# Optimization experiments

Hardware: AMD Instinct MI355X
Metric: run time of the kernel (lower is better)

The kernel has to match this reference:

```python
import jax, jax.numpy as jnp
import numpy as np

N = 200000
E = 500000
F_IN = 165
HID = 256
N_CLASSES = 2


def setup_inputs() -> dict:
    key = jax.random.key(0)
    ks = jax.random.split(key, 8)
    x = jax.random.normal(ks[0], (N, F_IN), dtype=jnp.float32)
    edge_index = jax.random.randint(ks[1], (2, E), 0, N, dtype=jnp.int64)
    # PyG SAGEConv params: lin_l applied to mean-aggregated neighbors (with bias),
    # lin_r applied to root features (no bias). Glorot-ish init scale.
    def lin(k, fin, fout):
        return jax.random.normal(k, (fin, fout), dtype=jnp.float32) / np.sqrt(fin)
    return {
        "x": x,
        "edge_index": edge_index,
        "w1_l": lin(ks[2], F_IN, HID),
        "w1_r": lin(ks[3], F_IN, HID),
        "b1": jnp.zeros((HID,), dtype=jnp.float32),
        "w2_l": lin(ks[4], HID, N_CLASSES),
        "w2_r": lin(ks[5], HID, N_CLASSES),
        "b2": jnp.zeros((N_CLASSES,), dtype=jnp.float32),
    }


def _sage_conv(x, edge_index, w_l, w_r, b):
    # PyG SAGEConv with default mean aggregation:
    #   out = lin_l(mean_{j in N(i)} x_j) + lin_r(x_i) + b
    src, dst = edge_index[0], edge_index[1]
    n = x.shape[0]
    deg = jax.ops.segment_sum(jnp.ones((src.shape[0],), x.dtype), dst, num_segments=n)
    agg = jax.ops.segment_sum(x[src], dst, num_segments=n)  # [N, F]
    agg = agg / jnp.maximum(deg, 1.0)[:, None]
    return agg @ w_l + x @ w_r + b


def reference(x, edge_index, w1_l, w1_r, b1, w2_l, w2_r, b2):
    h = jax.nn.relu(_sage_conv(x, edge_index, w1_l, w1_r, b1))
    # F.dropout(training=self.training) is identity in eval mode.
    logits = _sage_conv(h, edge_index, w2_l, w2_r, b2)
    return (logits, edge_index)
```

## Files before the change

kernel.cpp:

```cpp
#include <hip/hip_runtime.h>
#include <hip/hip_bf16.h>
#include <hip/hip_fp16.h>

#define N_NODES 200000
#define N_EDGES 500000
#define F_IN    165
#define HID     256
#define SX      192
#define NB      782

typedef float    floatx4 __attribute__((ext_vector_type(4)));
typedef float    floatx4a __attribute__((ext_vector_type(4), aligned(16)));
typedef float    float4u __attribute__((ext_vector_type(4), aligned(4)));
typedef _Float16 half8   __attribute__((ext_vector_type(8)));

__global__ void cast_x_kernel(const float* __restrict__ x, half8* __restrict__ xh8) {
    int idx = blockIdx.x * blockDim.x + threadIdx.x;
    int row = idx / 24;
    int p = idx - row * 24;
    int f0 = p * 8;
    const float* px = x + (long)row * F_IN + f0;
    half8 r;
    if (f0 + 8 <= F_IN) {
        float4u lo = *(const float4u*)px;
        float4u hi = *(const float4u*)(px + 4);
#pragma unroll
        for (int q = 0; q < 4; ++q) r[q] = (_Float16)lo[q];
#pragma unroll
        for (int q = 0; q < 4; ++q) r[4 + q] = (_Float16)hi[q];
    } else {
#pragma unroll
        for (int q = 0; q < 8; ++q)
            r[q] = (f0 + q < F_IN) ? (_Float16)px[q] : (_Float16)0.0f;
    }
    xh8[idx] = r;
}

__global__ void hist_kernel(const int* __restrict__ ei, int* __restrict__ degi) {
    int e = blockIdx.x * blockDim.x + threadIdx.x;
    if (e < N_EDGES) atomicAdd(&degi[ei[N_EDGES + e]], 1);
}

__global__ __launch_bounds__(256) void block_sum_kernel(const int* __restrict__ degi,
                                                        int* __restrict__ bsum) {
    __shared__ int sh[256];
    int t = threadIdx.x, i = blockIdx.x * 256 + t;
    sh[t] = (i < N_NODES) ? degi[i] : 0;
    __syncthreads();
#pragma unroll
    for (int off = 128; off > 0; off >>= 1) {
        if (t < off) sh[t] += sh[t + off];
        __syncthreads();
    }
    if (t == 0) bsum[blockIdx.x] = sh[0];
}

__global__ __launch_bounds__(1024) void scan_bsum_kernel(const int* __restrict__ bsum,
                                                         int* __restrict__ boff,
                                                         int* __restrict__ row_start) {
    __shared__ int sh[1024];
    int t = threadIdx.x;
    int v = (t < NB) ? bsum[t] : 0;
    sh[t] = v;
    __syncthreads();
    for (int off = 1; off < 1024; off <<= 1) {
        int u = (t >= off) ? sh[t - off] : 0;
        __syncthreads();
        sh[t] += u;
        __syncthreads();
    }
    if (t < NB) boff[t] = sh[t] - v;
    if (t == 1023) row_start[N_NODES] = sh[1023];
}

__global__ __launch_bounds__(256) void scan_emit_kernel(const int* __restrict__ degi,
                                                        const int* __restrict__ boff,
                                                        int* __restrict__ row_start,
                                                        int* __restrict__ cursor,
                                                        float* __restrict__ invdeg) {
    __shared__ int sh[256];
    int t = threadIdx.x, i = blockIdx.x * 256 + t;
    int d = (i < N_NODES) ? degi[i] : 0;
    sh[t] = d;
    __syncthreads();
#pragma unroll
    for (int off = 1; off < 256; off <<= 1) {
        int u = (t >= off) ? sh[t - off] : 0;
        __syncthreads();
        sh[t] += u;
        __syncthreads();
    }
    if (i < N_NODES) {
        int row = boff[blockIdx.x] + sh[t] - d;
        row_start[i] = row;
        cursor[i] = row;
        invdeg[i] = 1.0f / fmaxf((float)d, 1.0f);
    }
}

__global__ void scatter_edges_kernel(const int* __restrict__ ei,
                                     int* __restrict__ cursor,
                                     int* __restrict__ csr) {
    int e = blockIdx.x * blockDim.x + threadIdx.x;
    if (e >= N_EDGES) return;
    int s = ei[e];
    int d = ei[N_EDGES + e];
    int pos = atomicAdd(&cursor[d], 1);
    csr[pos] = s;
}

__global__ void gather_agg_kernel(const half8* __restrict__ xh8,
                                  const int* __restrict__ row_start,
                                  const int* __restrict__ csr,
                                  half8* __restrict__ aggh8) {
    int idx = blockIdx.x * blockDim.x + threadIdx.x;
    int n = idx / 24;
    int p = idx - n * 24;
    int e0 = row_start[n], e1 = row_start[n + 1];
    half8 acc = {0, 0, 0, 0, 0, 0, 0, 0};
    half8 acc2 = {0, 0, 0, 0, 0, 0, 0, 0};
    int e = e0;
    for (; e + 2 <= e1; e += 2) {
        int s0 = csr[e], s1 = csr[e + 1];
        half8 v0 = xh8[(long)s0 * 24 + p];
        half8 v1 = xh8[(long)s1 * 24 + p];
        acc += v0;
        acc2 += v1;
    }
    if (e < e1) acc += xh8[(long)csr[e] * 24 + p];
    aggh8[idx] = acc + acc2;
}

__global__ void prep_bfrag_kernel(const float* __restrict__ w1l,
                                  const float* __restrict__ w1r,
                                  _Float16* __restrict__ bfrag) {
    int gid = blockIdx.x * blockDim.x + threadIdx.x;
    if (gid >= 12 * 16 * 64) return;
    int lane = gid & 63;
    int j = (gid >> 6) & 15;
    int c = gid >> 10;
    int quad = lane >> 4, n = lane & 15;
    const float* w = (c < 6) ? w1l : w1r;
    int kb = (c < 6 ? c : c - 6) * 32;
    int col = j * 16 + n;
    half8 r;
#pragma unroll
    for (int q = 0; q < 8; ++q) {
        int k = kb + quad * 8 + q;
        r[q] = (_Float16)((k < F_IN) ? w[k * HID + col] : 0.0f);
    }
    *(half8*)(bfrag + gid * 8) = r;
}

__global__ __launch_bounds__(512, 2) void gemm_fused_kernel(
        const _Float16* __restrict__ xh, const _Float16* __restrict__ aggh,
        const float* __restrict__ invdeg, const _Float16* __restrict__ bfrag,
        const float* __restrict__ b1,
        const float* __restrict__ w2l, const float* __restrict__ w2r,
        float* __restrict__ tl, float* __restrict__ tr) {
    __shared__ __attribute__((aligned(16))) _Float16 As[2][128 * 32];
    __shared__ float tlr[128][4];
    const int tid = threadIdx.x;
    const int w = tid >> 6, lane = tid & 63;
    const int quad = lane >> 4, l15 = lane & 15;
    const int rowbase = blockIdx.x * 128;
    const int mrow0 = rowbase + (w & 1) * 64;
    const int rhalf = (w & 1) * 64;
    const int jbase = (w >> 1) * 4;

    ((float*)tlr)[tid < 512 ? tid : 0] = 0.0f;

    const int srow_l = tid >> 2;
    const int sseg = (tid & 3) ^ ((srow_l >> 1) & 3);
    int srow = rowbase + srow_l;
    if (srow >= N_NODES) srow = N_NODES - 1;
    const long sgoff = (long)srow * SX + sseg * 8;

    floatx4 acc[4][4];
#pragma unroll
    for (int i = 0; i < 4; ++i)
#pragma unroll
        for (int jj = 0; jj < 4; ++jj)
            acc[i][jj] = (floatx4){0.f, 0.f, 0.f, 0.f};

    __syncthreads();

#pragma unroll 1
    for (int it = 0; it < 6; ++it) {
#pragma unroll
        for (int u = 0; u < 2; ++u) {
            const int cc = it * 2 + u;
            const _Float16* __restrict__ src = (cc < 6) ? aggh : xh;
            const int kb = (cc < 6 ? cc : cc - 6) * 32;
            const _Float16* gp = src + sgoff + kb;
            char* dst = (char*)(&As[u][0]) + (tid & ~63) * 16;
            __builtin_amdgcn_global_load_lds(
                (const __attribute__((address_space(1))) void*)gp,
                (__attribute__((address_space(3))) void*)dst, 16, 0, 0);
        }
        __syncthreads();

#pragma unroll
        for (int u = 0; u < 2; ++u) {
            const int cc = it * 2 + u;
            half8 a[4], b[4];
#pragma unroll
            for (int i = 0; i < 4; ++i) {
                int r = rhalf + i * 16 + l15;
                int slot = r * 4 + (quad ^ ((r >> 1) & 3));
                a[i] = *(const half8*)(&As[u][slot * 8]);
            }
#pragma unroll
            for (int jj = 0; jj < 4; ++jj)
                b[jj] = *(const half8*)(bfrag + (((cc * 16) + jbase + jj) * 64 + lane) * 8);
#pragma unroll
            for (int i = 0; i < 4; ++i)
#pragma unroll
                for (int jj = 0; jj < 4; ++jj)
                    acc[i][jj] = __builtin_amdgcn_mfma_f32_16x16x32_f16(a[i], b[jj], acc[i][jj], 0, 0, 0);

            if (cc == 5) {
#pragma unroll
                for (int i = 0; i < 4; ++i) {
                    int rb = mrow0 + i * 16 + quad * 4;
                    floatx4 iv;
                    if (rb + 3 < N_NODES) {
                        iv = *(const floatx4a*)(invdeg + rb);
                    } else {
#pragma unroll
                        for (int t = 0; t < 4; ++t)
                            iv[t] = (rb + t < N_NODES) ? invdeg[rb + t] : 0.0f;
                    }
#pragma unroll
                    for (int jj = 0; jj < 4; ++jj)
                        acc[i][jj] *= iv;
                }
            }
        }
        __syncthreads();
    }

    float bb[4], wl0[4], wl1[4], wr0[4], wr1[4];
#pragma unroll
    for (int jj = 0; jj < 4; ++jj) {
        int col = (w >> 1) * 64 + jj * 16 + l15;
        bb[jj]  = b1[col];
        wl0[jj] = w2l[col * 2];  wl1[jj] = w2l[col * 2 + 1];
        wr0[jj] = w2r[col * 2];  wr1[jj] = w2r[col * 2 + 1];
    }
#pragma unroll
    for (int i = 0; i < 4; ++i) {
#pragma unroll
        for (int t = 0; t < 4; ++t) {
            float s0 = 0.f, s1 = 0.f, s2 = 0.f, s3 = 0.f;
#pragma unroll
            for (int jj = 0; jj < 4; ++jj) {
                float v = fmaxf(acc[i][jj][t] + bb[jj], 0.0f);
                s0 += v * wl0[jj]; s1 += v * wl1[jj];
                s2 += v * wr0[jj]; s3 += v * wr1[jj];
            }
#pragma unroll
            for (int m = 1; m < 16; m <<= 1) {
                s0 += __shfl_xor(s0, m, 64);
                s1 += __shfl_xor(s1, m, 64);
                s2 += __shfl_xor(s2, m, 64);
                s3 += __shfl_xor(s3, m, 64);
            }
            if (l15 == 0) {
                int rl = (w & 1) * 64 + i * 16 + quad * 4 + t;
                atomicAdd(&tlr[rl][0], s0);
                atomicAdd(&tlr[rl][1], s1);
                atomicAdd(&tlr[rl][2], s2);
                atomicAdd(&tlr[rl][3], s3);
            }
        }
    }
    __syncthreads();
    if (tid < 128) {
        int row = rowbase + tid;
        if (row < N_NODES) {
            tl[row * 2 + 0] = tlr[tid][0];
            tl[row * 2 + 1] = tlr[tid][1];
            tr[row * 2 + 0] = tlr[tid][2];
            tr[row * 2 + 1] = tlr[tid][3];
        }
    }
}

__global__ void gather_out_kernel(const int* __restrict__ row_start,
                                  const int* __restrict__ csr,
                                  const float* __restrict__ tl,
                                  const float* __restrict__ tr,
                                  const float* __restrict__ invdeg,
                                  const float* __restrict__ b2,
                                  float* __restrict__ out) {
    int i = blockIdx.x * blockDim.x + threadIdx.x;
    if (i >= N_NODES) return;
    int e0 = row_start[i], e1 = row_start[i + 1];
    float a0 = 0.f, a1 = 0.f;
    for (int e = e0; e < e1; ++e) {
        int s = csr[e];
        a0 += tl[s * 2 + 0];
        a1 += tl[s * 2 + 1];
    }
    float inv = invdeg[i];
    out[i * 2 + 0] = a0 * inv + tr[i * 2 + 0] + b2[0];
    out[i * 2 + 1] = a1 * inv + tr[i * 2 + 1] + b2[1];
}

__global__ void cast_edges_kernel(const int* __restrict__ ei,
                                  float* __restrict__ out) {
    int i = blockIdx.x * blockDim.x + threadIdx.x;
    if (i < 2 * N_EDGES) out[i] = (float)ei[i];
}

extern "C" void kernel_launch(void* const* d_in, const int* in_sizes, int n_in,
                              void* d_out, int out_size, void* d_ws, size_t ws_size,
                              hipStream_t stream) {
    const float* x    = (const float*)d_in[0];
    const int*   ei   = (const int*)d_in[1];
    const float* w1_l = (const float*)d_in[2];
    const float* w1_r = (const float*)d_in[3];
    const float* b1   = (const float*)d_in[4];
    const float* w2_l = (const float*)d_in[5];
    const float* w2_r = (const float*)d_in[6];
    const float* b2   = (const float*)d_in[7];

    char* ws = (char*)d_ws;
    int*   degi      = (int*)(ws);
    int*   row_start = (int*)(ws + 800000);
    int*   cursor    = (int*)(ws + 1600032);
    float* invdeg    = (float*)(ws + 2400032);
    int*   csr       = (int*)(ws + 3200032);
    float* tl        = (float*)(ws + 5200032);
    float* tr        = (float*)(ws + 6800032);
    int*   bsum      = (int*)(ws + 8400032);
    int*   boff      = (int*)(ws + 8403232);
    _Float16* bfrag  = (_Float16*)(ws + 8406432);
    _Float16* aggh   = (_Float16*)(ws + 8610000);
    _Float16* xh     = (_Float16*)(ws + 85410000);

    float* out = (float*)d_out;

    (void)hipMemsetAsync(degi, 0, 800000, stream);

    cast_x_kernel<<<(N_NODES * 24) / 256, 256, 0, stream>>>(x, (half8*)xh);
    prep_bfrag_kernel<<<48, 256, 0, stream>>>(w1_l, w1_r, bfrag);

    hist_kernel<<<(N_EDGES + 255) / 256, 256, 0, stream>>>(ei, degi);
    block_sum_kernel<<<NB, 256, 0, stream>>>(degi, bsum);
    scan_bsum_kernel<<<1, 1024, 0, stream>>>(bsum, boff, row_start);
    scan_emit_kernel<<<NB, 256, 0, stream>>>(degi, boff, row_start, cursor, invdeg);
    scatter_edges_kernel<<<(N_EDGES + 255) / 256, 256, 0, stream>>>(ei, cursor, csr);

    gather_agg_kernel<<<(N_NODES * 24) / 256, 256, 0, stream>>>(
        (const half8*)xh, row_start, csr, (half8*)aggh);

    gemm_fused_kernel<<<(N_NODES + 127) / 128, 512, 0, stream>>>(
        xh, aggh, invdeg, bfrag, b1, w2_l, w2_r, tl, tr);

    gather_out_kernel<<<NB, 256, 0, stream>>>(row_start, csr, tl, tr, invdeg, b2, out);
    cast_edges_kernel<<<(2 * N_EDGES + 255) / 256, 256, 0, stream>>>(ei, out + 2 * N_NODES);
}
```

Before: 427.0 us.

## Fuse neighbor gather-mean into layer-1 GEMM and merge edge cast with histogram

The separate gather_agg kernel, along with its fp16 aggregate buffer, is removed. Each GEMM block now gathers neighbor rows for its 128 nodes directly into LDS, scaled by inverse degree. This is interleaved with async loads of the root features, so the gather overlaps MFMA work on the lin_r half, and the weight fragment order is swapped to match. The edge-index float cast is also fused with the degree histogram in one pass. The cost is more LDS per block (which may lower occupancy), and the irregular gather now runs inside the GEMM with a possible load imbalance across waves.

```diff
diff --git a/kernel.cpp b/kernel.cpp
--- a/kernel.cpp
+++ b/kernel.cpp
@@ -6,11 +6,9 @@
 #define N_EDGES 500000
 #define F_IN    165
 #define HID     256
-#define SX      192
 #define NB      782
 
 typedef float    floatx4 __attribute__((ext_vector_type(4)));
-typedef float    floatx4a __attribute__((ext_vector_type(4), aligned(16)));
 typedef float    float4u __attribute__((ext_vector_type(4), aligned(4)));
 typedef _Float16 half8   __attribute__((ext_vector_type(8)));
 
@@ -36,9 +34,14 @@
     xh8[idx] = r;
 }
 
-__global__ void hist_kernel(const int* __restrict__ ei, int* __restrict__ degi) {
-    int e = blockIdx.x * blockDim.x + threadIdx.x;
-    if (e < N_EDGES) atomicAdd(&degi[ei[N_EDGES + e]], 1);
+__global__ void cast_edges_hist_kernel(const int* __restrict__ ei,
+                                       float* __restrict__ oute,
+                                       int* __restrict__ degi) {
+    int i = blockIdx.x * blockDim.x + threadIdx.x;
+    if (i >= 2 * N_EDGES) return;
+    int v = ei[i];
+    oute[i] = (float)v;
+    if (i >= N_EDGES) atomicAdd(&degi[v], 1);
 }
 
 __global__ __launch_bounds__(256) void block_sum_kernel(const int* __restrict__ degi,
@@ -109,28 +112,6 @@
     csr[pos] = s;
 }
 
-__global__ void gather_agg_kernel(const half8* __restrict__ xh8,
-                                  const int* __restrict__ row_start,
-                                  const int* __restrict__ csr,
-                                  half8* __restrict__ aggh8) {
-    int idx = blockIdx.x * blockDim.x + threadIdx.x;
-    int n = idx / 24;
-    int p = idx - n * 24;
-    int e0 = row_start[n], e1 = row_start[n + 1];
-    half8 acc = {0, 0, 0, 0, 0, 0, 0, 0};
-    half8 acc2 = {0, 0, 0, 0, 0, 0, 0, 0};
-    int e = e0;
-    for (; e + 2 <= e1; e += 2) {
-        int s0 = csr[e], s1 = csr[e + 1];
-        half8 v0 = xh8[(long)s0 * 24 + p];
-        half8 v1 = xh8[(long)s1 * 24 + p];
-        acc += v0;
-        acc2 += v1;
-    }
-    if (e < e1) acc += xh8[(long)csr[e] * 24 + p];
-    aggh8[idx] = acc + acc2;
-}
-
 __global__ void prep_bfrag_kernel(const float* __restrict__ w1l,
                                   const float* __restrict__ w1r,
                                   _Float16* __restrict__ bfrag) {
@@ -140,7 +121,7 @@
     int j = (gid >> 6) & 15;
     int c = gid >> 10;
     int quad = lane >> 4, n = lane & 15;
-    const float* w = (c < 6) ? w1l : w1r;
+    const float* w = (c < 6) ? w1r : w1l;
     int kb = (c < 6 ? c : c - 6) * 32;
     int col = j * 16 + n;
     half8 r;
@@ -153,28 +134,39 @@
 }
 
 __global__ __launch_bounds__(512, 2) void gemm_fused_kernel(
-        const _Float16* __restrict__ xh, const _Float16* __restrict__ aggh,
+        const half8* __restrict__ xh8,
+        const int* __restrict__ row_start, const int* __restrict__ csr,
         const float* __restrict__ invdeg, const _Float16* __restrict__ bfrag,
         const float* __restrict__ b1,
         const float* __restrict__ w2l, const float* __restrict__ w2r,
         float* __restrict__ tl, float* __restrict__ tr) {
-    __shared__ __attribute__((aligned(16))) _Float16 As[2][128 * 32];
+    __shared__ __attribute__((aligned(16))) _Float16 X[4][128 * 32];
+    __shared__ __attribute__((aligned(16))) _Float16 G[4][128 * 32];
     __shared__ float tlr[128][4];
+    const _Float16* xh = (const _Float16*)xh8;
     const int tid = threadIdx.x;
     const int w = tid >> 6, lane = tid & 63;
     const int quad = lane >> 4, l15 = lane & 15;
     const int rowbase = blockIdx.x * 128;
-    const int mrow0 = rowbase + (w & 1) * 64;
     const int rhalf = (w & 1) * 64;
     const int jbase = (w >> 1) * 4;
 
-    ((float*)tlr)[tid < 512 ? tid : 0] = 0.0f;
-
-    const int srow_l = tid >> 2;
-    const int sseg = (tid & 3) ^ ((srow_l >> 1) & 3);
-    int srow = rowbase + srow_l;
-    if (srow >= N_NODES) srow = N_NODES - 1;
-    const long sgoff = (long)srow * SX + sseg * 8;
+    ((float*)tlr)[tid] = 0.0f;
+
+    const int row_l = tid >> 2;
+    const int sfetch = (tid & 3) ^ ((row_l >> 1) & 3);
+    const int grow = rowbase + row_l;
+    const bool growv = grow < N_NODES;
+    const int srow = growv ? grow : (N_NODES - 1);
+
+    int ge0 = 0, ge1 = 0;
+    float ginv = 0.0f;
+    if (growv) {
+        ge0 = row_start[grow];
+        ge1 = row_start[grow + 1];
+        ginv = invdeg[grow];
+    }
+    const int gslot_b = (row_l * 4 + sfetch) * 16;
 
     floatx4 acc[4][4];
 #pragma unroll
@@ -183,61 +175,71 @@
         for (int jj = 0; jj < 4; ++jj)
             acc[i][jj] = (floatx4){0.f, 0.f, 0.f, 0.f};
 
-    __syncthreads();
-
-#pragma unroll 1
-    for (int it = 0; it < 6; ++it) {
-#pragma unroll
-        for (int u = 0; u < 2; ++u) {
-            const int cc = it * 2 + u;
-            const _Float16* __restrict__ src = (cc < 6) ? aggh : xh;
-            const int kb = (cc < 6 ? cc : cc - 6) * 32;
-            const _Float16* gp = src + sgoff + kb;
-            char* dst = (char*)(&As[u][0]) + (tid & ~63) * 16;
-            __builtin_amdgcn_global_load_lds(
-                (const __attribute__((address_space(1))) void*)gp,
-                (__attribute__((address_space(3))) void*)dst, 16, 0, 0);
+    auto issue = [&](int c, int buf) {
+        const _Float16* gp = xh + ((long)srow * 24 + c * 4 + sfetch) * 8;
+        char* dst = (char*)(&X[buf][0]) + (tid & ~63) * 16;
+        __builtin_amdgcn_global_load_lds(
+            (const __attribute__((address_space(1))) void*)gp,
+            (__attribute__((address_space(3))) void*)dst, 16, 0, 0);
+    };
+
+    auto gather = [&](int ac, int buf) {
+        half8 a0 = {0, 0, 0, 0, 0, 0, 0, 0};
+        half8 a1 = {0, 0, 0, 0, 0, 0, 0, 0};
+        const long segoff = ac * 4 + sfetch;
+        int e = ge0;
+        for (; e + 2 <= ge1; e += 2) {
+            int s0 = csr[e], s1 = csr[e + 1];
+            a0 += xh8[(long)s0 * 24 + segoff];
+            a1 += xh8[(long)s1 * 24 + segoff];
         }
-        __syncthreads();
-
-#pragma unroll
-        for (int u = 0; u < 2; ++u) {
-            const int cc = it * 2 + u;
-            half8 a[4], b[4];
-#pragma unroll
-            for (int i = 0; i < 4; ++i) {
-                int r = rhalf + i * 16 + l15;
-                int slot = r * 4 + (quad ^ ((r >> 1) & 3));
-                a[i] = *(const half8*)(&As[u][slot * 8]);
-            }
+        if (e < ge1) a0 += xh8[(long)csr[e] * 24 + segoff];
+        a0 += a1;
+        half8 r;
+#pragma unroll
+        for (int q = 0; q < 8; ++q) r[q] = (_Float16)((float)a0[q] * ginv);
+        *(half8*)((char*)(&G[buf][0]) + gslot_b) = r;
+    };
+
+    auto compute = [&](const _Float16* buf, int cc) {
+        half8 a[4], b[4];
+#pragma unroll
+        for (int i = 0; i < 4; ++i) {
+            int r = rhalf + i * 16 + l15;
+            int slot = r * 4 + (quad ^ ((r >> 1) & 3));
+            a[i] = *(const half8*)(buf + slot * 8);
+        }
+#pragma unroll
+        for (int jj = 0; jj < 4; ++jj)
+            b[jj] = *(const half8*)(bfrag + (((cc * 16) + jbase + jj) * 64 + lane) * 8);
+#pragma unroll
+        for (int i = 0; i < 4; ++i)
 #pragma unroll
             for (int jj = 0; jj < 4; ++jj)
-                b[jj] = *(const half8*)(bfrag + (((cc * 16) + jbase + jj) * 64 + lane) * 8);
-#pragma unroll
-            for (int i = 0; i < 4; ++i)
-#pragma unroll
-                for (int jj = 0; jj < 4; ++jj)
-                    acc[i][jj] = __builtin_amdgcn_mfma_f32_16x16x32_f16(a[i], b[jj], acc[i][jj], 0, 0, 0);
-
-            if (cc == 5) {
-#pragma unroll
-                for (int i = 0; i < 4; ++i) {
-                    int rb = mrow0 + i * 16 + quad * 4;
-                    floatx4 iv;
-                    if (rb + 3 < N_NODES) {
-                        iv = *(const floatx4a*)(invdeg + rb);
-                    } else {
-#pragma unroll
-                        for (int t = 0; t < 4; ++t)
-                            iv[t] = (rb + t < N_NODES) ? invdeg[rb + t] : 0.0f;
-                    }
-#pragma unroll
-                    for (int jj = 0; jj < 4; ++jj)
-                        acc[i][jj] *= iv;
-                }
-            }
-        }
-        __syncthreads();
+                acc[i][jj] = __builtin_amdgcn_mfma_f32_16x16x32_f16(a[i], b[jj], acc[i][jj], 0, 0, 0);
+    };
+
+    issue(0, 0); issue(1, 1);
+    gather(0, 0);
+    __syncthreads();
+    issue(2, 2); issue(3, 3);
+    compute(&X[0][0], 0); compute(&X[1][0], 1);
+    gather(1, 1);
+    __syncthreads();
+    issue(4, 0); issue(5, 1);
+    compute(&X[2][0], 2); compute(&X[3][0], 3);
+    gather(2, 2);
+    __syncthreads();
+    compute(&X[0][0], 4); compute(&X[1][0], 5);
+    gather(3, 3);
+    __syncthreads();
+
+#pragma unroll
+    for (int ac = 0; ac < 6; ++ac) {
+        compute(&G[ac & 3][0], 6 + ac);
+        __syncthreads();
+        if (ac == 0) gather(4, 0);
+        if (ac == 1) gather(5, 1);
     }
 
     float bb[4], wl0[4], wl1[4], wr0[4], wr1[4];
@@ -308,12 +310,6 @@
     out[i * 2 + 1] = a1 * inv + tr[i * 2 + 1] + b2[1];
 }
 
-__global__ void cast_edges_kernel(const int* __restrict__ ei,
-                                  float* __restrict__ out) {
-    int i = blockIdx.x * blockDim.x + threadIdx.x;
-    if (i < 2 * N_EDGES) out[i] = (float)ei[i];
-}
-
 extern "C" void kernel_launch(void* const* d_in, const int* in_sizes, int n_in,
                               void* d_out, int out_size, void* d_ws, size_t ws_size,
                               hipStream_t stream) {
@@ -337,28 +333,24 @@
     int*   bsum      = (int*)(ws + 8400032);
     int*   boff      = (int*)(ws + 8403232);
     _Float16* bfrag  = (_Float16*)(ws + 8406432);
-    _Float16* aggh   = (_Float16*)(ws + 8610000);
-    _Float16* xh     = (_Float16*)(ws + 85410000);
+    half8* xh8       = (half8*)(ws + 8610000);
 
     float* out = (float*)d_out;
 
     (void)hipMemsetAsync(degi, 0, 800000, stream);
 
-    cast_x_kernel<<<(N_NODES * 24) / 256, 256, 0, stream>>>(x, (half8*)xh);
+    cast_edges_hist_kernel<<<(2 * N_EDGES + 255) / 256, 256, 0, stream>>>(
+        ei, out + 2 * N_NODES, degi);
+    cast_x_kernel<<<(N_NODES * 24) / 256, 256, 0, stream>>>(x, xh8);
     prep_bfrag_kernel<<<48, 256, 0, stream>>>(w1_l, w1_r, bfrag);
 
-    hist_kernel<<<(N_EDGES + 255) / 256, 256, 0, stream>>>(ei, degi);
     block_sum_kernel<<<NB, 256, 0, stream>>>(degi, bsum);
     scan_bsum_kernel<<<1, 1024, 0, stream>>>(bsum, boff, row_start);
     scan_emit_kernel<<<NB, 256, 0, stream>>>(degi, boff, row_start, cursor, invdeg);
     scatter_edges_kernel<<<(N_EDGES + 255) / 256, 256, 0, stream>>>(ei, cursor, csr);
 
-    gather_agg_kernel<<<(N_NODES * 24) / 256, 256, 0, stream>>>(
-        (const half8*)xh, row_start, csr, (half8*)aggh);
-
     gemm_fused_kernel<<<(N_NODES + 127) / 128, 512, 0, stream>>>(
-        xh, aggh, invdeg, bfrag, b1, w2_l, w2_r, tl, tr);
+        xh8, row_start, csr, invdeg, bfrag, b1, w2_l, w2_r, tl, tr);
 
     gather_out_kernel<<<NB, 256, 0, stream>>>(row_start, csr, tl, tr, invdeg, b2, out);
-    cast_edges_kernel<<<(2 * N_EDGES + 255) / 256, 256, 0, stream>>>(ei, out + 2 * N_NODES);
-}
+}
```

Measured after the change: 487.3 us. 1.14x slower.
